# Optimization experiments

Hardware: AMD Instinct MI355X
Metric: run time of the kernel (lower is better)

## Reference

```python
import jax, jax.numpy as jnp
import numpy as np

DIM = 1024
HEADS = 16
DHEAD = DIM // HEADS

def setup_inputs() -> dict:
    key = jax.random.key(0)
    ks = jax.random.split(key, 7)
    b, n = 4, 2048
    x = jax.random.normal(ks[0], (b, n, DIM), dtype=jnp.float32)
    bias = jax.random.normal(ks[1], (HEADS, n, n), dtype=jnp.float32) * 0.02
    w_qkv = jax.random.normal(ks[2], (DIM, 3 * DIM), dtype=jnp.float32) * (DIM ** -0.5)
    w_out = jax.random.normal(ks[3], (DIM, DIM), dtype=jnp.float32) * (DIM ** -0.5)
    b_out = jax.random.normal(ks[4], (DIM,), dtype=jnp.float32) * 0.01
    ln_gamma = jnp.ones((DIM,), dtype=jnp.float32)
    ln_beta = jnp.zeros((DIM,), dtype=jnp.float32)
    return {"x": x, "relative_position_bias": bias, "w_qkv": w_qkv,
            "w_out": w_out, "b_out": b_out, "ln_gamma": ln_gamma, "ln_beta": ln_beta}

def reference(x, relative_position_bias, w_qkv, w_out, b_out, ln_gamma, ln_beta):
    # LayerNorm
    mu = jnp.mean(x, axis=-1, keepdims=True)
    var = jnp.var(x, axis=-1, keepdims=True)
    xn = (x - mu) * jax.lax.rsqrt(var + 1e-5) * ln_gamma + ln_beta
    # QKV projection (no bias)
    qkv = xn @ w_qkv  # [b, n, 3*dim]
    q, k, v = jnp.split(qkv, 3, axis=-1)
    b, n, _ = x.shape
    def heads(t):
        return t.reshape(b, n, HEADS, DHEAD).transpose(0, 2, 1, 3)  # b h n d
    q, k, v = heads(q), heads(k), heads(v)
    scale = DHEAD ** -0.5
    scores = jnp.einsum('bhid,bhjd->bhij', q, k) * scale + relative_position_bias
    attn = jax.nn.softmax(scores, axis=-1)
    out = jnp.einsum('bhij,bhjd->bhid', attn, v)
    out = out.transpose(0, 2, 1, 3).reshape(b, n, DIM)
    return out @ w_out + b_out
```

## Files before the change

kernel.cpp:

```cpp
#include <hip/hip_runtime.h>

typedef unsigned short u16;
typedef __attribute__((ext_vector_type(8))) short s8v;
typedef __attribute__((ext_vector_type(4))) float f4v;

#define MFMA16(a, b, c) __builtin_amdgcn_mfma_f32_16x16x32_bf16((a), (b), (c), 0, 0, 0)

#define GLOAD16(gp, lp) __builtin_amdgcn_global_load_lds(                      \
    (const __attribute__((address_space(1))) void*)(gp),                       \
    (__attribute__((address_space(3))) void*)(lp), 16, 0, 0)

__device__ inline float bf2f(u16 h) { return __uint_as_float(((unsigned)h) << 16); }
__device__ inline u16 f2bf(float f) {
    unsigned u = __float_as_uint(f);
    u += 0x7FFFu + ((u >> 16) & 1u);
    return (u16)(u >> 16);
}

__global__ void probe_kernel(const u16* __restrict__ x16, int* __restrict__ flag) {
    int lane = threadIdx.x;
    int cnt = 0;
    for (int i = lane; i < 2048; i += 64) {
        float v = bf2f(x16[2 * i]);
        float a = fabsf(v);
        bool sane = (a == 0.0f) || (a > 1e-5f && a < 1e5f);
        if (!sane) cnt++;
    }
#pragma unroll
    for (int off = 32; off; off >>= 1) cnt += __shfl_xor(cnt, off);
    if (lane == 0) flag[0] = (cnt > 512) ? 1 : 0;
}

__global__ __launch_bounds__(256) void transpose_convert_kernel(
    const void* __restrict__ src, u16* __restrict__ dst,
    const int* __restrict__ flagp, int K, int N) {
    __shared__ float t[32][33];
    int f = *flagp;
    int n0 = blockIdx.x * 32, k0 = blockIdx.y * 32;
    int tid = threadIdx.x;
    int r = tid >> 3, c4 = (tid & 7) * 4;
    if (f) {
        const float* s = (const float*)src + (size_t)(k0 + r) * N + n0 + c4;
        float4 v = *(const float4*)s;
        t[r][c4] = v.x; t[r][c4 + 1] = v.y; t[r][c4 + 2] = v.z; t[r][c4 + 3] = v.w;
    } else {
        const u16* s = (const u16*)src + (size_t)(k0 + r) * N + n0 + c4;
        uint2 v = *(const uint2*)s;
        t[r][c4]     = bf2f((u16)(v.x & 0xffff));
        t[r][c4 + 1] = bf2f((u16)(v.x >> 16));
        t[r][c4 + 2] = bf2f((u16)(v.y & 0xffff));
        t[r][c4 + 3] = bf2f((u16)(v.y >> 16));
    }
    __syncthreads();
    u16 o[4];
#pragma unroll
    for (int i = 0; i < 4; i++) o[i] = f2bf(t[c4 + i][r]);
    uint2 packed;
    packed.x = (unsigned)o[0] | ((unsigned)o[1] << 16);
    packed.y = (unsigned)o[2] | ((unsigned)o[3] << 16);
    *(uint2*)(dst + (size_t)(n0 + r) * K + k0 + c4) = packed;
}

__global__ __launch_bounds__(256) void ln_kernel(const void* __restrict__ xv,
                                                 const void* __restrict__ gv,
                                                 const void* __restrict__ bv,
                                                 u16* __restrict__ xn,
                                                 const int* __restrict__ flagp) {
    int f = *flagp;
    int row = blockIdx.x;
    int tid = threadIdx.x;
    int lane = tid & 63, wave = tid >> 6;

    float v[4];
    if (f) {
        const float* xr = (const float*)xv + (size_t)row * 1024;
        float4 a = ((const float4*)xr)[tid];
        v[0] = a.x; v[1] = a.y; v[2] = a.z; v[3] = a.w;
    } else {
        const u16* xr = (const u16*)xv + (size_t)row * 1024;
        uint2 raw = ((const uint2*)xr)[tid];
        v[0] = bf2f((u16)(raw.x & 0xffff));
        v[1] = bf2f((u16)(raw.x >> 16));
        v[2] = bf2f((u16)(raw.y & 0xffff));
        v[3] = bf2f((u16)(raw.y >> 16));
    }

    float s = v[0] + v[1] + v[2] + v[3];
    float ss = v[0]*v[0] + v[1]*v[1] + v[2]*v[2] + v[3]*v[3];
#pragma unroll
    for (int off = 32; off; off >>= 1) {
        s  += __shfl_xor(s, off);
        ss += __shfl_xor(ss, off);
    }
    __shared__ float red[8];
    if (lane == 0) { red[wave] = s; red[4 + wave] = ss; }
    __syncthreads();
    s  = red[0] + red[1] + red[2] + red[3];
    ss = red[4] + red[5] + red[6] + red[7];

    float mu  = s * (1.0f / 1024.0f);
    float var = ss * (1.0f / 1024.0f) - mu * mu;
    float rs  = rsqrtf(var + 1e-5f);

    u16 o[4];
#pragma unroll
    for (int i = 0; i < 4; i++) {
        int c = tid * 4 + i;
        float g = f ? ((const float*)gv)[c] : bf2f(((const u16*)gv)[c]);
        float b = f ? ((const float*)bv)[c] : bf2f(((const u16*)bv)[c]);
        float y = (v[i] - mu) * rs * g + b;
        o[i] = f2bf(y);
    }
    uint2 packed;
    packed.x = (unsigned)o[0] | ((unsigned)o[1] << 16);
    packed.y = (unsigned)o[2] | ((unsigned)o[3] << 16);
    ((uint2*)(xn + (size_t)row * 1024))[tid] = packed;
}

template <int MODE>
__global__ __launch_bounds__(256) void gemm_kernel(const u16* __restrict__ A,
                                                   const u16* __restrict__ WT,
                                                   const void* __restrict__ bias,
                                                   const int* __restrict__ flagp,
                                                   void* __restrict__ outv,
                                                   int M, int N, int K) {
    __shared__ __align__(16) u16 As[128 * 64];
    __shared__ __align__(16) u16 Bs[128 * 64];

    int tid = threadIdx.x;
    int lane = tid & 63, wave = tid >> 6;
    int quad = lane >> 4, l16 = lane & 15;
    int wr = wave >> 1, wc = wave & 1;
    int m0 = blockIdx.y * 128, n0 = blockIdx.x * 128;

    int srow = lane >> 3;
    int sk   = (lane & 7) * 8;
    const u16* pa = A  + (size_t)(m0 + wave * 32 + srow) * K + sk;
    const u16* pb = WT + (size_t)(n0 + wave * 32 + srow) * K + sk;

    f4v acc[4][4];
#pragma unroll
    for (int i = 0; i < 4; i++)
#pragma unroll
        for (int j = 0; j < 4; j++) acc[i][j] = (f4v){0.f, 0.f, 0.f, 0.f};

    for (int k0 = 0; k0 < K; k0 += 64) {
        __syncthreads();
#pragma unroll
        for (int cs = 0; cs < 4; cs++) {
            GLOAD16(pa + (size_t)cs * 8 * K + k0, &As[(wave * 32 + cs * 8) * 64]);
            GLOAD16(pb + (size_t)cs * 8 * K + k0, &Bs[(wave * 32 + cs * 8) * 64]);
        }
        __syncthreads();

#pragma unroll
        for (int kc = 0; kc < 2; kc++) {
            s8v afr[4], bfr[4];
#pragma unroll
            for (int mi = 0; mi < 4; mi++)
                afr[mi] = *(const s8v*)&As[(wr * 64 + mi * 16 + l16) * 64 + kc * 32 + quad * 8];
#pragma unroll
            for (int ni = 0; ni < 4; ni++)
                bfr[ni] = *(const s8v*)&Bs[(wc * 64 + ni * 16 + l16) * 64 + kc * 32 + quad * 8];
#pragma unroll
            for (int mi = 0; mi < 4; mi++)
#pragma unroll
                for (int ni = 0; ni < 4; ni++)
                    acc[mi][ni] = MFMA16(afr[mi], bfr[ni], acc[mi][ni]);
        }
    }

    int f = (MODE == 1) ? *flagp : 0;

#pragma unroll
    for (int mi = 0; mi < 4; mi++) {
#pragma unroll
        for (int ni = 0; ni < 4; ni++) {
#pragma unroll
            for (int r = 0; r < 4; r++) {
                int gm = m0 + wr * 64 + mi * 16 + quad * 4 + r;
                int gn = n0 + wc * 64 + ni * 16 + l16;
                float v = acc[mi][ni][r];
                if (MODE == 1) {
                    float bb = f ? ((const float*)bias)[gn]
                                 : bf2f(((const u16*)bias)[gn]);
                    ((float*)outv)[(size_t)gm * N + gn] = v + bb;
                } else {
                    u16* out = (u16*)outv;
                    int sel = gn >> 10, rem = gn & 1023;
                    int h = rem >> 6, d = rem & 63;
                    int b = gm >> 11, q = gm & 2047;
                    size_t dst;
                    if (sel == 2)
                        dst = ((size_t)(b * 16 + h) * 64 + d) * 2048 + q;
                    else
                        dst = ((size_t)(b * 16 + h) * 2048 + q) * 64 + d;
                    out[(size_t)sel * 8388608 + dst] = f2bf(v);
                }
            }
        }
    }
}

__global__ __launch_bounds__(256) void attn_kernel(const u16* __restrict__ qg,
                                                   const u16* __restrict__ kg,
                                                   const u16* __restrict__ vtg,
                                                   const void* __restrict__ bias,
                                                   const int* __restrict__ flagp,
                                                   u16* __restrict__ out) {
    int d_ = blockIdx.x;
    int xcd = d_ & 7, t_ = d_ >> 3;
    int b = t_ & 3;
    int g = (t_ >> 2) * 8 + xcd;
    int h = g & 15, qt = g >> 4;
    int q0 = qt * 64;
    int bh = b * 16 + h;
    int f = *flagp;

    int tid = threadIdx.x;
    int lane = tid & 63, wave = tid >> 6;
    int quad = lane >> 4, l16 = lane & 15;

    __shared__ __align__(16) u16 Ks[64][72];
    __shared__ __align__(16) u16 Vt[64][72];
    __shared__ __align__(16) u16 Ps[4][16][72];

    const u16* qrow = qg + ((size_t)bh * 2048 + q0 + wave * 16 + l16) * 64;
    s8v qf0 = *(const s8v*)(qrow + quad * 8);
    s8v qf1 = *(const s8v*)(qrow + 32 + quad * 8);

    f4v oacc[4];
#pragma unroll
    for (int i = 0; i < 4; i++) oacc[i] = (f4v){0.f, 0.f, 0.f, 0.f};
    float mrow[4] = {-1e30f, -1e30f, -1e30f, -1e30f};
    float lrow[4] = {0.f, 0.f, 0.f, 0.f};

    const u16* kbase = kg + (size_t)bh * 2048 * 64;
    const u16* vbase = vtg + (size_t)bh * 64 * 2048;
    size_t boff = ((size_t)h * 2048 + q0 + wave * 16 + quad * 4) * 2048;
    const float* bbf = (const float*)bias + boff;
    const u16*   bbh = (const u16*)bias + boff;

    for (int kt = 0; kt < 2048; kt += 64) {
        __syncthreads();
#pragma unroll
        for (int c = tid; c < 512; c += 256) {
            int row = c >> 3, c8 = (c & 7) * 8;
            *(uint4*)&Ks[row][c8] = *(const uint4*)(kbase + (size_t)(kt + row) * 64 + c8);
            *(uint4*)&Vt[row][c8] = *(const uint4*)(vbase + (size_t)row * 2048 + kt + c8);
        }
        __syncthreads();

        f4v sc[4];
#pragma unroll
        for (int ni = 0; ni < 4; ni++) {
            s8v k0f = *(const s8v*)&Ks[ni * 16 + l16][quad * 8];
            s8v k1f = *(const s8v*)&Ks[ni * 16 + l16][32 + quad * 8];
            f4v t = (f4v){0.f, 0.f, 0.f, 0.f};
            t = MFMA16(qf0, k0f, t);
            t = MFMA16(qf1, k1f, t);
            sc[ni] = t;
        }

        float barr[4][4];
        if (f) {
#pragma unroll
            for (int r = 0; r < 4; r++)
#pragma unroll
                for (int ni = 0; ni < 4; ni++)
                    barr[ni][r] = bbf[(size_t)r * 2048 + kt + ni * 16 + l16];
        } else {
#pragma unroll
            for (int r = 0; r < 4; r++)
#pragma unroll
                for (int ni = 0; ni < 4; ni++)
                    barr[ni][r] = bf2f(bbh[(size_t)r * 2048 + kt + ni * 16 + l16]);
        }
        float sv[4][4];
#pragma unroll
        for (int r = 0; r < 4; r++)
#pragma unroll
            for (int ni = 0; ni < 4; ni++)
                sv[ni][r] = sc[ni][r] * 0.125f + barr[ni][r];

        float mx[4];
#pragma unroll
        for (int r = 0; r < 4; r++) {
            mx[r] = fmaxf(fmaxf(sv[0][r], sv[1][r]), fmaxf(sv[2][r], sv[3][r]));
#pragma unroll
            for (int off = 1; off < 16; off <<= 1)
                mx[r] = fmaxf(mx[r], __shfl_xor(mx[r], off));
        }
        float alpha[4], rsum[4];
#pragma unroll
        for (int r = 0; r < 4; r++) {
            float mnew = fmaxf(mrow[r], mx[r]);
            alpha[r] = __expf(mrow[r] - mnew);
            mrow[r] = mnew;
            rsum[r] = 0.f;
#pragma unroll
            for (int ni = 0; ni < 4; ni++) {
                float p = __expf(sv[ni][r] - mnew);
                rsum[r] += p;
                Ps[wave][quad * 4 + r][ni * 16 + l16] = f2bf(p);
            }
        }
#pragma unroll
        for (int r = 0; r < 4; r++) {
#pragma unroll
            for (int off = 1; off < 16; off <<= 1)
                rsum[r] += __shfl_xor(rsum[r], off);
            lrow[r] = lrow[r] * alpha[r] + rsum[r];
        }
#pragma unroll
        for (int od = 0; od < 4; od++) {
            f4v t = oacc[od];
            t[0] *= alpha[0]; t[1] *= alpha[1]; t[2] *= alpha[2]; t[3] *= alpha[3];
            oacc[od] = t;
        }
        __syncthreads();

        s8v pf0 = *(const s8v*)&Ps[wave][l16][quad * 8];
        s8v pf1 = *(const s8v*)&Ps[wave][l16][32 + quad * 8];
#pragma unroll
        for (int od = 0; od < 4; od++) {
            s8v vf0 = *(const s8v*)&Vt[od * 16 + l16][quad * 8];
            s8v vf1 = *(const s8v*)&Vt[od * 16 + l16][32 + quad * 8];
            oacc[od] = MFMA16(pf0, vf0, oacc[od]);
            oacc[od] = MFMA16(pf1, vf1, oacc[od]);
        }
    }

    float inv[4];
#pragma unroll
    for (int r = 0; r < 4; r++) inv[r] = 1.0f / lrow[r];
#pragma unroll
    for (int od = 0; od < 4; od++) {
#pragma unroll
        for (int r = 0; r < 4; r++) {
            size_t dst = ((size_t)b * 2048 + q0 + wave * 16 + quad * 4 + r) * 1024 +
                         h * 64 + od * 16 + l16;
            out[dst] = f2bf(oacc[od][r] * inv[r]);
        }
    }
}

extern "C" void kernel_launch(void* const* d_in, const int* in_sizes, int n_in,
                              void* d_out, int out_size, void* d_ws, size_t ws_size,
                              hipStream_t stream) {
    const void* x      = d_in[0];
    const void* bias   = d_in[1];
    const void* w_qkv  = d_in[2];
    const void* w_out  = d_in[3];
    const void* b_out  = d_in[4];
    const void* gamma  = d_in[5];
    const void* beta   = d_in[6];

    u16* base = (u16*)d_ws;
    int* flag = (int*)d_ws;
    u16* xn   = base + 64;
    u16* qkv  = xn + 8388608;
    u16* attn = qkv + 3 * 8388608;
    u16* wqT  = attn + 8388608;
    u16* woT  = wqT + 3145728;

    probe_kernel<<<dim3(1), dim3(64), 0, stream>>>((const u16*)x, flag);

    ln_kernel<<<dim3(8192), dim3(256), 0, stream>>>(x, gamma, beta, xn, flag);

    transpose_convert_kernel<<<dim3(96, 32), dim3(256), 0, stream>>>(
        w_qkv, wqT, flag, 1024, 3072);
    transpose_convert_kernel<<<dim3(32, 32), dim3(256), 0, stream>>>(
        w_out, woT, flag, 1024, 1024);

    gemm_kernel<0><<<dim3(3072 / 128, 8192 / 128), dim3(256), 0, stream>>>(
        xn, wqT, nullptr, flag, qkv, 8192, 3072, 1024);

    attn_kernel<<<dim3(2048), dim3(256), 0, stream>>>(
        qkv, qkv + 8388608, qkv + 2 * 8388608, bias, flag, attn);

    gemm_kernel<1><<<dim3(1024 / 128, 8192 / 128), dim3(256), 0, stream>>>(
        attn, woT, b_out, flag, d_out, 8192, 1024, 1024);
}
```

Before: 751.3 us.

## Write V row-major, add separate transpose, use swizzled direct-to-LDS K/V loads

The QKV GEMM epilogue now writes V in the same row-major head layout as Q and K. This replaces its strided, uncoalesced transposed scatter, and a small tiled kernel then transposes V into the free xn buffer. The attention kernel loads K and V^T tiles with global_load_lds into an XOR-swizzled, unpadded LDS layout and reads them back with matching swizzled addresses. It also drops the barrier before the per-wave P reads. This adds an extra kernel launch and a round trip of V through memory, in exchange for coalesced writes and asynchronous LDS fills.

```diff
diff --git a/kernel.cpp b/kernel.cpp
--- a/kernel.cpp
+++ b/kernel.cpp
@@ -61,6 +61,25 @@
     *(uint2*)(dst + (size_t)(n0 + r) * K + k0 + c4) = packed;
 }
 
+__global__ __launch_bounds__(256) void transpose_v_kernel(const u16* __restrict__ v,
+                                                          u16* __restrict__ vt) {
+    __shared__ u16 t[64][72];
+    int bh = blockIdx.y;
+    int n0 = blockIdx.x * 64;
+    int tid = threadIdx.x;
+    int r = tid >> 2, c = (tid & 3) * 16;
+    const u16* src = v + ((size_t)bh * 2048 + n0 + r) * 64 + c;
+    *(uint4*)&t[r][c]     = *(const uint4*)src;
+    *(uint4*)&t[r][c + 8] = *(const uint4*)(src + 8);
+    __syncthreads();
+    u16 o[16];
+#pragma unroll
+    for (int i = 0; i < 16; i++) o[i] = t[c + i][r];
+    u16* dst = vt + ((size_t)bh * 64 + r) * 2048 + n0 + c;
+    *(uint4*)dst       = *(const uint4*)&o[0];
+    *(uint4*)(dst + 8) = *(const uint4*)&o[8];
+}
+
 __global__ __launch_bounds__(256) void ln_kernel(const void* __restrict__ xv,
                                                  const void* __restrict__ gv,
                                                  const void* __restrict__ bv,
@@ -190,11 +209,7 @@
                     int sel = gn >> 10, rem = gn & 1023;
                     int h = rem >> 6, d = rem & 63;
                     int b = gm >> 11, q = gm & 2047;
-                    size_t dst;
-                    if (sel == 2)
-                        dst = ((size_t)(b * 16 + h) * 64 + d) * 2048 + q;
-                    else
-                        dst = ((size_t)(b * 16 + h) * 2048 + q) * 64 + d;
+                    size_t dst = ((size_t)(b * 16 + h) * 2048 + q) * 64 + d;
                     out[(size_t)sel * 8388608 + dst] = f2bf(v);
                 }
             }
@@ -221,8 +236,8 @@
     int lane = tid & 63, wave = tid >> 6;
     int quad = lane >> 4, l16 = lane & 15;
 
-    __shared__ __align__(16) u16 Ks[64][72];
-    __shared__ __align__(16) u16 Vt[64][72];
+    __shared__ __align__(16) u16 Ks[64 * 64];
+    __shared__ __align__(16) u16 Vt[64 * 64];
     __shared__ __align__(16) u16 Ps[4][16][72];
 
     const u16* qrow = qg + ((size_t)bh * 2048 + q0 + wave * 16 + l16) * 64;
@@ -237,25 +252,36 @@
 
     const u16* kbase = kg + (size_t)bh * 2048 * 64;
     const u16* vbase = vtg + (size_t)bh * 64 * 2048;
+
+    int srow = lane >> 3;
+    int scol = ((lane & 7) ^ srow) * 16;
+    const char* kp = (const char*)kbase + ((size_t)(wave * 16 + srow)) * 128 + scol;
+    const char* vp = (const char*)vbase + ((size_t)(wave * 16 + srow)) * 4096 + scol;
+    u16* ksl = &Ks[wave * 16 * 64];
+    u16* vsl = &Vt[wave * 16 * 64];
+
+    int xr = (l16 & 7) << 4;
+
     size_t boff = ((size_t)h * 2048 + q0 + wave * 16 + quad * 4) * 2048;
     const float* bbf = (const float*)bias + boff;
     const u16*   bbh = (const u16*)bias + boff;
 
     for (int kt = 0; kt < 2048; kt += 64) {
         __syncthreads();
-#pragma unroll
-        for (int c = tid; c < 512; c += 256) {
-            int row = c >> 3, c8 = (c & 7) * 8;
-            *(uint4*)&Ks[row][c8] = *(const uint4*)(kbase + (size_t)(kt + row) * 64 + c8);
-            *(uint4*)&Vt[row][c8] = *(const uint4*)(vbase + (size_t)row * 2048 + kt + c8);
-        }
+        GLOAD16(kp, ksl);
+        GLOAD16(kp + 1024, ksl + 512);
+        GLOAD16(vp, vsl);
+        GLOAD16(vp + 8 * 4096, vsl + 512);
+        kp += 64 * 128;
+        vp += 128;
         __syncthreads();
 
         f4v sc[4];
 #pragma unroll
         for (int ni = 0; ni < 4; ni++) {
-            s8v k0f = *(const s8v*)&Ks[ni * 16 + l16][quad * 8];
-            s8v k1f = *(const s8v*)&Ks[ni * 16 + l16][32 + quad * 8];
+            const char* krow = (const char*)Ks + (ni * 16 + l16) * 128;
+            s8v k0f = *(const s8v*)(krow + ((quad * 16) ^ xr));
+            s8v k1f = *(const s8v*)(krow + ((64 + quad * 16) ^ xr));
             f4v t = (f4v){0.f, 0.f, 0.f, 0.f};
             t = MFMA16(qf0, k0f, t);
             t = MFMA16(qf1, k1f, t);
@@ -318,14 +344,14 @@
             t[0] *= alpha[0]; t[1] *= alpha[1]; t[2] *= alpha[2]; t[3] *= alpha[3];
             oacc[od] = t;
         }
-        __syncthreads();
 
         s8v pf0 = *(const s8v*)&Ps[wave][l16][quad * 8];
         s8v pf1 = *(const s8v*)&Ps[wave][l16][32 + quad * 8];
 #pragma unroll
         for (int od = 0; od < 4; od++) {
-            s8v vf0 = *(const s8v*)&Vt[od * 16 + l16][quad * 8];
-            s8v vf1 = *(const s8v*)&Vt[od * 16 + l16][32 + quad * 8];
+            const char* vrow = (const char*)Vt + (od * 16 + l16) * 128;
+            s8v vf0 = *(const s8v*)(vrow + ((quad * 16) ^ xr));
+            s8v vf1 = *(const s8v*)(vrow + ((64 + quad * 16) ^ xr));
             oacc[od] = MFMA16(pf0, vf0, oacc[od]);
             oacc[od] = MFMA16(pf1, vf1, oacc[od]);
         }
@@ -376,8 +402,11 @@
     gemm_kernel<0><<<dim3(3072 / 128, 8192 / 128), dim3(256), 0, stream>>>(
         xn, wqT, nullptr, flag, qkv, 8192, 3072, 1024);
 
+    transpose_v_kernel<<<dim3(32, 64), dim3(256), 0, stream>>>(
+        qkv + 2 * 8388608, xn);
+
     attn_kernel<<<dim3(2048), dim3(256), 0, stream>>>(
-        qkv, qkv + 8388608, qkv + 2 * 8388608, bias, flag, attn);
+        qkv, qkv + 8388608, xn, bias, flag, attn);
 
     gemm_kernel<1><<<dim3(1024 / 128, 8192 / 128), dim3(256), 0, stream>>>(
         attn, woT, b_out, flag, d_out, 8192, 1024, 1024);
```

After: 719.8 us. 1.04x faster.
